# Kernel optimization log

Hardware: AMD Instinct MI355X
Metric: run time of the kernel (lower is better)

Reference implementation:

```python
import jax, jax.numpy as jnp
import numpy as np

B, S, D, H = 2, 4096, 512, 8
DK = D // H  # 64

def setup_inputs() -> dict:
    key = jax.random.key(0)
    k1, k2, k3, k4 = jax.random.split(key, 4)
    return {
        "queries": jax.random.normal(k1, (B, S, D), dtype=jnp.float32),
        "keys": jax.random.normal(k2, (B, S, D), dtype=jnp.float32),
        "values": jax.random.normal(k3, (B, S, D), dtype=jnp.float32),
        "W_o": jax.random.normal(k4, (D, D), dtype=jnp.float32) * (1.0 / np.sqrt(D)),
        "b_o": jnp.zeros((D,), dtype=jnp.float32),
    }

def reference(queries, keys, values, W_o, b_o):
    b_s, nq, _ = queries.shape
    nk = keys.shape[1]
    # split heads: (b, s, h, dk) -> (b, h, s, dk)
    q = queries.reshape(b_s, nq, H, DK).transpose(0, 2, 1, 3)
    k = keys.reshape(b_s, nk, H, DK).transpose(0, 2, 1, 3)
    v = values.reshape(b_s, nk, H, DK).transpose(0, 2, 1, 3)
    # full (nq, nk) attention matrix, scaled by sqrt(d_k)
    att = jnp.einsum("bhqd,bhkd->bhqk", q, k) / np.sqrt(DK).astype(np.float32)
    att = jax.nn.softmax(att, axis=-1)  # dropout is identity at inference
    out = jnp.einsum("bhqk,bhkd->bhqd", att, v)
    out = out.transpose(0, 2, 1, 3).reshape(b_s, nq, H * DK)
    return out @ W_o + b_o
```

## Files before the change

### kernel.cpp

```cpp
#include <hip/hip_runtime.h>
#include <hip/hip_bf16.h>

#define Bn 2
#define Sn 4096
#define Dn 512
#define Hn 8

typedef _Float16 f16x8 __attribute__((ext_vector_type(8)));
typedef __fp16 fp16x2 __attribute__((ext_vector_type(2)));
typedef float f32x16 __attribute__((ext_vector_type(16)));
typedef unsigned uint2v __attribute__((ext_vector_type(2)));

#if __has_builtin(__builtin_amdgcn_global_load_lds)
#define HAS_GLL 1
typedef const __attribute__((address_space(1))) unsigned int* gas1_t;
typedef __attribute__((address_space(3))) unsigned int* las3_t;
static __device__ __forceinline__ void ld_lds16(const void* g, void* l) {
    __builtin_amdgcn_global_load_lds((gas1_t)g, (las3_t)l, 16, 0, 0);
}
#else
#define HAS_GLL 0
#endif

static __device__ __forceinline__ unsigned pkh(float a, float b) {
    union { fp16x2 h; unsigned u; } r;
    r.h = __builtin_amdgcn_cvt_pkrtz(a, b);
    return r.u;
}

static __device__ __forceinline__ f16x8 xchg2(unsigned g0x, unsigned g0y,
                                              unsigned g1x, unsigned g1y, int hi) {
    union { unsigned u[4]; f16x8 v; } f;
#if __has_builtin(__builtin_amdgcn_permlane32_swap)
    uint2v rx = __builtin_amdgcn_permlane32_swap(g0x, g1x, false, false);
    uint2v ry = __builtin_amdgcn_permlane32_swap(g0y, g1y, false, false);
    f.u[0] = rx.x; f.u[1] = ry.x; f.u[2] = rx.y; f.u[3] = ry.y;
#else
    int sx = hi ? (int)g0x : (int)g1x;
    int sy = hi ? (int)g0y : (int)g1y;
    int rx = __shfl_xor(sx, 32);
    int ry = __shfl_xor(sy, 32);
    unsigned ox = hi ? g1x : g0x;
    unsigned oy = hi ? g1y : g0y;
    f.u[0] = hi ? (unsigned)rx : ox;
    f.u[1] = hi ? (unsigned)ry : oy;
    f.u[2] = hi ? ox : (unsigned)rx;
    f.u[3] = hi ? oy : (unsigned)ry;
#endif
    return f.v;
}

__global__ __launch_bounds__(256) void prep_kernel(
    const float* __restrict__ K, const float* __restrict__ V, const float* __restrict__ W,
    unsigned short* __restrict__ Kb, unsigned short* __restrict__ Vb,
    unsigned short* __restrict__ Wb) {
    const int vb = blockIdx.x;
    const int tid = threadIdx.x;
    if (vb < 1024) {
        const int kt = vb & 63, bh = vb >> 6;
        const int b = bh >> 3, h = bh & 7;
        unsigned short* dst = Kb + ((size_t)bh * 64 + kt) * 4096;
#pragma unroll
        for (int i = 0; i < 2; ++i) {
            int c = tid + i * 256;
            int f = c >> 6, ln = c & 63;
            int ktile = f >> 2, ks = f & 3;
            int row = ktile * 32 + (ln & 31);
            int dk = ks * 16 + (ln >> 5) * 8;
            const float* src = K + ((size_t)(b * Sn + kt * 64 + row)) * Dn + h * 64 + dk;
            float4 a0 = *(const float4*)src;
            float4 a1 = *(const float4*)(src + 4);
            uint4 o;
            o.x = pkh(a0.x, a0.y); o.y = pkh(a0.z, a0.w);
            o.z = pkh(a1.x, a1.y); o.w = pkh(a1.z, a1.w);
            *(uint4*)(dst + c * 8) = o;
        }
    } else if (vb < 2048) {
        const int u = vb - 1024;
        const int kt = u & 63, bh = u >> 6;
        const int b = bh >> 3, h = bh & 7;
        unsigned short* dst = Vb + ((size_t)bh * 64 + kt) * 4096;
#pragma unroll
        for (int i = 0; i < 2; ++i) {
            int c = tid + i * 256;
            int f = c >> 6, ln = c & 63;
            int dt = f >> 2, ks = f & 3;
            int dk = dt * 32 + (ln & 31);
            int key0 = ks * 16 + (ln >> 5) * 8;
            const float* src = V + ((size_t)(b * Sn + kt * 64 + key0)) * Dn + h * 64 + dk;
            uint4 o;
            o.x = pkh(src[0 * Dn], src[1 * Dn]);
            o.y = pkh(src[2 * Dn], src[3 * Dn]);
            o.z = pkh(src[4 * Dn], src[5 * Dn]);
            o.w = pkh(src[6 * Dn], src[7 * Dn]);
            *(uint4*)(dst + c * 8) = o;
        }
    } else {
        int c = (vb - 2048) * 256 + tid;
        int ln = c & 63, f = c >> 6;
        int ntile = f >> 5, ks = f & 31;
        int n = ntile * 32 + (ln & 31);
        int k0 = ks * 16 + (ln >> 5) * 8;
        uint4 o;
        o.x = pkh(W[(size_t)(k0 + 0) * Dn + n], W[(size_t)(k0 + 1) * Dn + n]);
        o.y = pkh(W[(size_t)(k0 + 2) * Dn + n], W[(size_t)(k0 + 3) * Dn + n]);
        o.z = pkh(W[(size_t)(k0 + 4) * Dn + n], W[(size_t)(k0 + 5) * Dn + n]);
        o.w = pkh(W[(size_t)(k0 + 6) * Dn + n], W[(size_t)(k0 + 7) * Dn + n]);
        *(uint4*)(Wb + c * 8) = o;
    }
}

__global__ __launch_bounds__(256, 2) void attn_kernel(
    const float* __restrict__ Q,
    const unsigned short* __restrict__ Kb,
    const unsigned short* __restrict__ Vb,
    unsigned short* __restrict__ ObA) {
    __shared__ __align__(16) unsigned short KV[32768];

    const int qt = blockIdx.x;
    const int bh = blockIdx.y;
    const int b = bh >> 3, h = bh & 7;
    const int tid = threadIdx.x;
    const int wg = tid >> 6;
    const int half = wg >> 1;
    const int qs = wg & 1;
    const int lane = tid & 63;
    const int q = lane & 31;
    const int hi = lane >> 5;
    const float cexp = 0.18033688f;

    f16x8 qf0[4], qf1[4];
    {
        const float* qp0 = Q + ((size_t)(b * Sn + qt * 128 + qs * 64 + q)) * Dn + h * 64 + hi * 8;
        const float* qp1 = qp0 + (size_t)32 * Dn;
#pragma unroll
        for (int ks = 0; ks < 4; ++ks) {
            float4 a0 = *(const float4*)(qp0 + ks * 16);
            float4 a1 = *(const float4*)(qp0 + ks * 16 + 4);
            union { unsigned u[4]; f16x8 v; } f;
            f.u[0] = pkh(a0.x * cexp, a0.y * cexp);
            f.u[1] = pkh(a0.z * cexp, a0.w * cexp);
            f.u[2] = pkh(a1.x * cexp, a1.y * cexp);
            f.u[3] = pkh(a1.z * cexp, a1.w * cexp);
            qf0[ks] = f.v;
            a0 = *(const float4*)(qp1 + ks * 16);
            a1 = *(const float4*)(qp1 + ks * 16 + 4);
            f.u[0] = pkh(a0.x * cexp, a0.y * cexp);
            f.u[1] = pkh(a0.z * cexp, a0.w * cexp);
            f.u[2] = pkh(a1.x * cexp, a1.y * cexp);
            f.u[3] = pkh(a1.z * cexp, a1.w * cexp);
            qf1[ks] = f.v;
        }
    }

    f32x16 zf;
#pragma unroll
    for (int r = 0; r < 16; ++r) zf[r] = 0.f;
    f32x16 oacc[2][2];
    oacc[0][0] = zf; oacc[0][1] = zf; oacc[1][0] = zf; oacc[1][1] = zf;
    float l0_ = 0.f, l1_ = 0.f;

    const size_t tbase = ((size_t)bh * 64 + half * 32) * 4096;
    const unsigned short* sgw = (qs ? Vb : Kb) + tbase;
    unsigned short* const lbase = &KV[half * 8192 + qs * 4096];

#if HAS_GLL
#define STAGE(itx, bb) { \
    const unsigned short* sp = sgw + (size_t)(itx) * 4096 + lane * 8; \
    unsigned short* ld = lbase + (bb) * 16384; \
    _Pragma("unroll") \
    for (int c = 0; c < 8; ++c) ld_lds16(sp + c * 512, ld + c * 512); }
#else
#define STAGE(itx, bb) { \
    const unsigned short* sp = sgw + (size_t)(itx) * 4096 + lane * 8; \
    unsigned short* ld = lbase + (bb) * 16384; \
    _Pragma("unroll") \
    for (int c = 0; c < 8; ++c) { \
        uint4 a = *(const uint4*)(sp + c * 512); \
        *(uint4*)&ld[c * 512 + lane * 8] = a; } }
#endif

    STAGE(0, 0);

    for (int it = 0; it < 32; ++it) {
        __syncthreads();
        const unsigned short* Kbuf = &KV[(it & 1) * 16384 + half * 8192];
        const unsigned short* Vbuf = Kbuf + 4096;
        if (it < 31) STAGE(it + 1, (it + 1) & 1);

#pragma unroll
        for (int kt2 = 0; kt2 < 2; ++kt2) {
            f32x16 sa0, sa1;
            {
                f16x8 kf = *(const f16x8*)&Kbuf[(kt2 * 4 + 0) * 512 + lane * 8];
                sa0 = __builtin_amdgcn_mfma_f32_32x32x16_f16(kf, qf0[0], zf, 0, 0, 0);
                sa1 = __builtin_amdgcn_mfma_f32_32x32x16_f16(kf, qf1[0], zf, 0, 0, 0);
#pragma unroll
                for (int ks = 1; ks < 4; ++ks) {
                    kf = *(const f16x8*)&Kbuf[(kt2 * 4 + ks) * 512 + lane * 8];
                    sa0 = __builtin_amdgcn_mfma_f32_32x32x16_f16(kf, qf0[ks], sa0, 0, 0, 0);
                    sa1 = __builtin_amdgcn_mfma_f32_32x32x16_f16(kf, qf1[ks], sa1, 0, 0, 0);
                }
            }
            unsigned u0[8], u1[8];
            float s0 = 0.f, s1 = 0.f;
#pragma unroll
            for (int j = 0; j < 8; ++j) {
                float ea = __builtin_amdgcn_exp2f(sa0[2 * j]);
                float eb = __builtin_amdgcn_exp2f(sa0[2 * j + 1]);
                s0 += ea + eb;
                u0[j] = pkh(ea, eb);
            }
#pragma unroll
            for (int j = 0; j < 8; ++j) {
                float ea = __builtin_amdgcn_exp2f(sa1[2 * j]);
                float eb = __builtin_amdgcn_exp2f(sa1[2 * j + 1]);
                s1 += ea + eb;
                u1[j] = pkh(ea, eb);
            }
            l0_ += s0; l1_ += s1;

#pragma unroll
            for (int kp = 0; kp < 2; ++kp) {
                f16x8 pb0 = xchg2(u0[4 * kp + 0], u0[4 * kp + 1], u0[4 * kp + 2], u0[4 * kp + 3], hi);
                f16x8 pb1 = xchg2(u1[4 * kp + 0], u1[4 * kp + 1], u1[4 * kp + 2], u1[4 * kp + 3], hi);
                f16x8 va0 = *(const f16x8*)&Vbuf[(0 * 4 + kt2 * 2 + kp) * 512 + lane * 8];
                f16x8 va1 = *(const f16x8*)&Vbuf[(1 * 4 + kt2 * 2 + kp) * 512 + lane * 8];
                oacc[0][0] = __builtin_amdgcn_mfma_f32_32x32x16_f16(va0, pb0, oacc[0][0], 0, 0, 0);
                oacc[0][1] = __builtin_amdgcn_mfma_f32_32x32x16_f16(va1, pb0, oacc[0][1], 0, 0, 0);
                oacc[1][0] = __builtin_amdgcn_mfma_f32_32x32x16_f16(va0, pb1, oacc[1][0], 0, 0, 0);
                oacc[1][1] = __builtin_amdgcn_mfma_f32_32x32x16_f16(va1, pb1, oacc[1][1], 0, 0, 0);
            }
        }
    }

    __syncthreads();
    float* red = (float*)KV + qs * 4224;
    if (half) {
#pragma unroll
        for (int t = 0; t < 2; ++t)
#pragma unroll
            for (int dt = 0; dt < 2; ++dt)
#pragma unroll
                for (int g = 0; g < 4; ++g) {
                    float4 v;
                    v.x = oacc[t][dt][g * 4 + 0];
                    v.y = oacc[t][dt][g * 4 + 1];
                    v.z = oacc[t][dt][g * 4 + 2];
                    v.w = oacc[t][dt][g * 4 + 3];
                    *(float4*)&red[((t * 2 + dt) * 4 + g) * 256 + lane * 4] = v;
                }
        red[4096 + lane] = l0_;
        red[4096 + 64 + lane] = l1_;
    }
    __syncthreads();
    if (!half) {
#pragma unroll
        for (int t = 0; t < 2; ++t)
#pragma unroll
            for (int dt = 0; dt < 2; ++dt)
#pragma unroll
                for (int g = 0; g < 4; ++g) {
                    float4 v = *(const float4*)&red[((t * 2 + dt) * 4 + g) * 256 + lane * 4];
                    oacc[t][dt][g * 4 + 0] += v.x;
                    oacc[t][dt][g * 4 + 1] += v.y;
                    oacc[t][dt][g * 4 + 2] += v.z;
                    oacc[t][dt][g * 4 + 3] += v.w;
                }
        l0_ += red[4096 + lane];
        l1_ += red[4096 + 64 + lane];
        l0_ += __shfl_xor(l0_, 32);
        l1_ += __shfl_xor(l1_, 32);
#pragma unroll
        for (int t = 0; t < 2; ++t) {
            const float li = 1.f / (t ? l1_ : l0_);
            const int gm = b * 128 + qt * 4 + qs * 2 + t;
#pragma unroll
            for (int ksg = 0; ksg < 4; ++ksg) {
                const int dt = ksg >> 1, k2 = ksg & 1;
                unsigned g0x = pkh(oacc[t][dt][8 * k2 + 0] * li, oacc[t][dt][8 * k2 + 1] * li);
                unsigned g0y = pkh(oacc[t][dt][8 * k2 + 2] * li, oacc[t][dt][8 * k2 + 3] * li);
                unsigned g1x = pkh(oacc[t][dt][8 * k2 + 4] * li, oacc[t][dt][8 * k2 + 5] * li);
                unsigned g1y = pkh(oacc[t][dt][8 * k2 + 6] * li, oacc[t][dt][8 * k2 + 7] * li);
                f16x8 frag = xchg2(g0x, g0y, g1x, g1y, hi);
                union { f16x8 v; uint4 u; } fu; fu.v = frag;
                *(uint4*)&ObA[((size_t)(gm * 32 + h * 4 + ksg) * 64 + lane) * 8] = fu.u;
            }
        }
    }
}

__global__ __launch_bounds__(256) void proj_kernel(
    const unsigned short* __restrict__ ObA,
    const unsigned short* __restrict__ Wb,
    const float* __restrict__ bias,
    float* __restrict__ out) {
    __shared__ __align__(16) unsigned short Ash[8192];
    __shared__ __align__(16) unsigned short Wsh[4096];

    const int mt = blockIdx.x;
    const int nt = blockIdx.y;
    const int tid = threadIdx.x;
    const int w = tid >> 6;
    const int lane = tid & 63;
    const int q = lane & 31;
    const int hi = lane >> 5;

    f32x16 acc[2];
#pragma unroll
    for (int t = 0; t < 2; ++t)
#pragma unroll
        for (int r = 0; r < 16; ++r) acc[t][r] = 0.f;

    for (int kt = 0; kt < 8; ++kt) {
        __syncthreads();
#pragma unroll
        for (int i = 0; i < 4; ++i) {
            int ci = (tid >> 6) + i * 4;
            int ml = ci >> 2, ksl = ci & 3;
            *(uint4*)&Ash[ci * 512 + lane * 8] =
                *(const uint4*)(ObA + (((size_t)(mt * 4 + ml) * 32 + kt * 4 + ksl) * 64 + lane) * 8);
        }
#pragma unroll
        for (int i = 0; i < 2; ++i) {
            int ci = (tid >> 6) + i * 4;
            int ntl = ci >> 2, ksl = ci & 3;
            *(uint4*)&Wsh[ci * 512 + lane * 8] =
                *(const uint4*)(Wb + (((size_t)(nt * 2 + ntl) * 32 + kt * 4 + ksl) * 64 + lane) * 8);
        }
        __syncthreads();

#pragma unroll
        for (int ks = 0; ks < 4; ++ks) {
            f16x8 a  = *(const f16x8*)&Ash[(w * 4 + ks) * 512 + lane * 8];
            f16x8 b0 = *(const f16x8*)&Wsh[(0 * 4 + ks) * 512 + lane * 8];
            f16x8 b1 = *(const f16x8*)&Wsh[(4 + ks) * 512 + lane * 8];
            acc[0] = __builtin_amdgcn_mfma_f32_32x32x16_f16(a, b0, acc[0], 0, 0, 0);
            acc[1] = __builtin_amdgcn_mfma_f32_32x32x16_f16(a, b1, acc[1], 0, 0, 0);
        }
    }

#pragma unroll
    for (int ntl = 0; ntl < 2; ++ntl) {
        int col = nt * 64 + ntl * 32 + q;
        float bv = bias[col];
#pragma unroll
        for (int reg = 0; reg < 16; ++reg) {
            int row = mt * 128 + w * 32 + (reg & 3) + 8 * (reg >> 2) + 4 * hi;
            out[(size_t)row * Dn + col] = acc[ntl][reg] + bv;
        }
    }
}

extern "C" void kernel_launch(void* const* d_in, const int* in_sizes, int n_in,
                              void* d_out, int out_size, void* d_ws, size_t ws_size,
                              hipStream_t stream) {
    const float* Q = (const float*)d_in[0];
    const float* K = (const float*)d_in[1];
    const float* V = (const float*)d_in[2];
    const float* W = (const float*)d_in[3];
    const float* bo = (const float*)d_in[4];
    float* out = (float*)d_out;

    char* ws = (char*)d_ws;
    unsigned short* Kb  = (unsigned short*)(ws);
    unsigned short* Vb  = (unsigned short*)(ws + 8388608);
    unsigned short* Wb  = (unsigned short*)(ws + 16777216);
    unsigned short* ObA = (unsigned short*)(ws + 17301504);

    prep_kernel<<<2176, 256, 0, stream>>>(K, V, W, Kb, Vb, Wb);
    attn_kernel<<<dim3(32, 16), 256, 0, stream>>>(Q, Kb, Vb, ObA);
    proj_kernel<<<dim3(64, 8), 256, 0, stream>>>(ObA, Wb, bo, out);
}
```

Baseline: 178.0 us.

## Split attention KV sequence across four wave pairs with 512-thread blocks

Doubles the attention block to 512 threads so that four key groups, instead of two, each process a quarter of the KV sequence for the same 128-query tile. Each iteration now handles 32 keys per group, and the partial outputs are reduced through LDS in two passes, one per query sub-tile, with extra barriers. Block indices are also remapped so consecutive blocks share query tiles across heads, and launch bounds ask for 4 blocks per CU. The aim is more waves in flight per CU to hide latency, at the cost of smaller MFMA batches per barrier and a larger reduction step.

```diff
diff --git a/kernel.cpp b/kernel.cpp
--- a/kernel.cpp
+++ b/kernel.cpp
@@ -110,19 +110,20 @@
     }
 }
 
-__global__ __launch_bounds__(256, 2) void attn_kernel(
+__global__ __launch_bounds__(512, 4) void attn_kernel(
     const float* __restrict__ Q,
     const unsigned short* __restrict__ Kb,
     const unsigned short* __restrict__ Vb,
     unsigned short* __restrict__ ObA) {
     __shared__ __align__(16) unsigned short KV[32768];
 
-    const int qt = blockIdx.x;
-    const int bh = blockIdx.y;
+    const int id = blockIdx.x + (blockIdx.y << 5);
+    const int qt = (id >> 3) & 31;
+    const int bh = (id & 7) + ((id >> 8) << 3);
     const int b = bh >> 3, h = bh & 7;
     const int tid = threadIdx.x;
     const int wg = tid >> 6;
-    const int half = wg >> 1;
+    const int kg = wg >> 1;
     const int qs = wg & 1;
     const int lane = tid & 63;
     const int q = lane & 31;
@@ -160,85 +161,101 @@
     oacc[0][0] = zf; oacc[0][1] = zf; oacc[1][0] = zf; oacc[1][1] = zf;
     float l0_ = 0.f, l1_ = 0.f;
 
-    const size_t tbase = ((size_t)bh * 64 + half * 32) * 4096;
-    const unsigned short* sgw = (qs ? Vb : Kb) + tbase;
-    unsigned short* const lbase = &KV[half * 8192 + qs * 4096];
+    const size_t bhbase = (size_t)bh * 64 * 4096;
 
 #if HAS_GLL
 #define STAGE(itx, bb) { \
-    const unsigned short* sp = sgw + (size_t)(itx) * 4096 + lane * 8; \
-    unsigned short* ld = lbase + (bb) * 16384; \
-    _Pragma("unroll") \
-    for (int c = 0; c < 8; ++c) ld_lds16(sp + c * 512, ld + c * 512); }
+    const int t64 = kg * 16 + ((itx) >> 1); \
+    const int lohi = (itx) & 1; \
+    unsigned short* dst = &KV[(bb) * 16384 + kg * 4096]; \
+    if (qs == 0) { \
+        const unsigned short* sp = Kb + bhbase + (size_t)t64 * 4096 + lohi * 2048 + lane * 8; \
+        ld_lds16(sp, dst); ld_lds16(sp + 512, dst + 512); \
+        ld_lds16(sp + 1024, dst + 1024); ld_lds16(sp + 1536, dst + 1536); \
+    } else { \
+        const unsigned short* sp = Vb + bhbase + (size_t)t64 * 4096 + lohi * 1024 + lane * 8; \
+        unsigned short* dv = dst + 2048; \
+        ld_lds16(sp, dv); ld_lds16(sp + 512, dv + 512); \
+        ld_lds16(sp + 2048, dv + 1024); ld_lds16(sp + 2560, dv + 1536); \
+    } }
 #else
 #define STAGE(itx, bb) { \
-    const unsigned short* sp = sgw + (size_t)(itx) * 4096 + lane * 8; \
-    unsigned short* ld = lbase + (bb) * 16384; \
-    _Pragma("unroll") \
-    for (int c = 0; c < 8; ++c) { \
-        uint4 a = *(const uint4*)(sp + c * 512); \
-        *(uint4*)&ld[c * 512 + lane * 8] = a; } }
+    const int t64 = kg * 16 + ((itx) >> 1); \
+    const int lohi = (itx) & 1; \
+    unsigned short* dst = &KV[(bb) * 16384 + kg * 4096]; \
+    if (qs == 0) { \
+        const unsigned short* sp = Kb + bhbase + (size_t)t64 * 4096 + lohi * 2048 + lane * 8; \
+        uint4 a0 = *(const uint4*)(sp); uint4 a1 = *(const uint4*)(sp + 512); \
+        uint4 a2 = *(const uint4*)(sp + 1024); uint4 a3 = *(const uint4*)(sp + 1536); \
+        *(uint4*)&dst[lane * 8] = a0; *(uint4*)&dst[512 + lane * 8] = a1; \
+        *(uint4*)&dst[1024 + lane * 8] = a2; *(uint4*)&dst[1536 + lane * 8] = a3; \
+    } else { \
+        const unsigned short* sp = Vb + bhbase + (size_t)t64 * 4096 + lohi * 1024 + lane * 8; \
+        unsigned short* dv = dst + 2048; \
+        uint4 a0 = *(const uint4*)(sp); uint4 a1 = *(const uint4*)(sp + 512); \
+        uint4 a2 = *(const uint4*)(sp + 2048); uint4 a3 = *(const uint4*)(sp + 2560); \
+        *(uint4*)&dv[lane * 8] = a0; *(uint4*)&dv[512 + lane * 8] = a1; \
+        *(uint4*)&dv[1024 + lane * 8] = a2; *(uint4*)&dv[1536 + lane * 8] = a3; \
+    } }
 #endif
 
     STAGE(0, 0);
 
     for (int it = 0; it < 32; ++it) {
         __syncthreads();
-        const unsigned short* Kbuf = &KV[(it & 1) * 16384 + half * 8192];
-        const unsigned short* Vbuf = Kbuf + 4096;
+        const unsigned short* Kbuf = &KV[(it & 1) * 16384 + kg * 4096];
+        const unsigned short* Vbuf = Kbuf + 2048;
         if (it < 31) STAGE(it + 1, (it + 1) & 1);
 
-#pragma unroll
-        for (int kt2 = 0; kt2 < 2; ++kt2) {
-            f32x16 sa0, sa1;
-            {
-                f16x8 kf = *(const f16x8*)&Kbuf[(kt2 * 4 + 0) * 512 + lane * 8];
-                sa0 = __builtin_amdgcn_mfma_f32_32x32x16_f16(kf, qf0[0], zf, 0, 0, 0);
-                sa1 = __builtin_amdgcn_mfma_f32_32x32x16_f16(kf, qf1[0], zf, 0, 0, 0);
-#pragma unroll
-                for (int ks = 1; ks < 4; ++ks) {
-                    kf = *(const f16x8*)&Kbuf[(kt2 * 4 + ks) * 512 + lane * 8];
-                    sa0 = __builtin_amdgcn_mfma_f32_32x32x16_f16(kf, qf0[ks], sa0, 0, 0, 0);
-                    sa1 = __builtin_amdgcn_mfma_f32_32x32x16_f16(kf, qf1[ks], sa1, 0, 0, 0);
-                }
+        f32x16 sa0, sa1;
+        {
+            f16x8 kf = *(const f16x8*)&Kbuf[0 * 512 + lane * 8];
+            sa0 = __builtin_amdgcn_mfma_f32_32x32x16_f16(kf, qf0[0], zf, 0, 0, 0);
+            sa1 = __builtin_amdgcn_mfma_f32_32x32x16_f16(kf, qf1[0], zf, 0, 0, 0);
+#pragma unroll
+            for (int ks = 1; ks < 4; ++ks) {
+                kf = *(const f16x8*)&Kbuf[ks * 512 + lane * 8];
+                sa0 = __builtin_amdgcn_mfma_f32_32x32x16_f16(kf, qf0[ks], sa0, 0, 0, 0);
+                sa1 = __builtin_amdgcn_mfma_f32_32x32x16_f16(kf, qf1[ks], sa1, 0, 0, 0);
             }
-            unsigned u0[8], u1[8];
-            float s0 = 0.f, s1 = 0.f;
-#pragma unroll
-            for (int j = 0; j < 8; ++j) {
-                float ea = __builtin_amdgcn_exp2f(sa0[2 * j]);
-                float eb = __builtin_amdgcn_exp2f(sa0[2 * j + 1]);
-                s0 += ea + eb;
-                u0[j] = pkh(ea, eb);
-            }
-#pragma unroll
-            for (int j = 0; j < 8; ++j) {
-                float ea = __builtin_amdgcn_exp2f(sa1[2 * j]);
-                float eb = __builtin_amdgcn_exp2f(sa1[2 * j + 1]);
-                s1 += ea + eb;
-                u1[j] = pkh(ea, eb);
-            }
-            l0_ += s0; l1_ += s1;
-
-#pragma unroll
-            for (int kp = 0; kp < 2; ++kp) {
-                f16x8 pb0 = xchg2(u0[4 * kp + 0], u0[4 * kp + 1], u0[4 * kp + 2], u0[4 * kp + 3], hi);
-                f16x8 pb1 = xchg2(u1[4 * kp + 0], u1[4 * kp + 1], u1[4 * kp + 2], u1[4 * kp + 3], hi);
-                f16x8 va0 = *(const f16x8*)&Vbuf[(0 * 4 + kt2 * 2 + kp) * 512 + lane * 8];
-                f16x8 va1 = *(const f16x8*)&Vbuf[(1 * 4 + kt2 * 2 + kp) * 512 + lane * 8];
-                oacc[0][0] = __builtin_amdgcn_mfma_f32_32x32x16_f16(va0, pb0, oacc[0][0], 0, 0, 0);
-                oacc[0][1] = __builtin_amdgcn_mfma_f32_32x32x16_f16(va1, pb0, oacc[0][1], 0, 0, 0);
-                oacc[1][0] = __builtin_amdgcn_mfma_f32_32x32x16_f16(va0, pb1, oacc[1][0], 0, 0, 0);
-                oacc[1][1] = __builtin_amdgcn_mfma_f32_32x32x16_f16(va1, pb1, oacc[1][1], 0, 0, 0);
-            }
+        }
+        unsigned u0[8], u1[8];
+        float s0 = 0.f, s1 = 0.f;
+#pragma unroll
+        for (int j = 0; j < 8; ++j) {
+            float ea = __builtin_amdgcn_exp2f(sa0[2 * j]);
+            float eb = __builtin_amdgcn_exp2f(sa0[2 * j + 1]);
+            s0 += ea + eb;
+            u0[j] = pkh(ea, eb);
+        }
+#pragma unroll
+        for (int j = 0; j < 8; ++j) {
+            float ea = __builtin_amdgcn_exp2f(sa1[2 * j]);
+            float eb = __builtin_amdgcn_exp2f(sa1[2 * j + 1]);
+            s1 += ea + eb;
+            u1[j] = pkh(ea, eb);
+        }
+        l0_ += s0; l1_ += s1;
+
+#pragma unroll
+        for (int ks2 = 0; ks2 < 2; ++ks2) {
+            f16x8 pb0 = xchg2(u0[4 * ks2 + 0], u0[4 * ks2 + 1], u0[4 * ks2 + 2], u0[4 * ks2 + 3], hi);
+            f16x8 pb1 = xchg2(u1[4 * ks2 + 0], u1[4 * ks2 + 1], u1[4 * ks2 + 2], u1[4 * ks2 + 3], hi);
+            f16x8 va0 = *(const f16x8*)&Vbuf[ks2 * 512 + lane * 8];
+            f16x8 va1 = *(const f16x8*)&Vbuf[1024 + ks2 * 512 + lane * 8];
+            oacc[0][0] = __builtin_amdgcn_mfma_f32_32x32x16_f16(va0, pb0, oacc[0][0], 0, 0, 0);
+            oacc[0][1] = __builtin_amdgcn_mfma_f32_32x32x16_f16(va1, pb0, oacc[0][1], 0, 0, 0);
+            oacc[1][0] = __builtin_amdgcn_mfma_f32_32x32x16_f16(va0, pb1, oacc[1][0], 0, 0, 0);
+            oacc[1][1] = __builtin_amdgcn_mfma_f32_32x32x16_f16(va1, pb1, oacc[1][1], 0, 0, 0);
         }
     }
 
     __syncthreads();
-    float* red = (float*)KV + qs * 4224;
-    if (half) {
-#pragma unroll
-        for (int t = 0; t < 2; ++t)
+    float* red = (float*)KV;
+#pragma unroll
+    for (int t = 0; t < 2; ++t) {
+        if (kg != 0) {
+            float* rp = red + (qs * 3 + (kg - 1)) * 2048;
 #pragma unroll
             for (int dt = 0; dt < 2; ++dt)
 #pragma unroll
@@ -248,27 +265,33 @@
                     v.y = oacc[t][dt][g * 4 + 1];
                     v.z = oacc[t][dt][g * 4 + 2];
                     v.w = oacc[t][dt][g * 4 + 3];
-                    *(float4*)&red[((t * 2 + dt) * 4 + g) * 256 + lane * 4] = v;
+                    *(float4*)&rp[(dt * 4 + g) * 256 + lane * 4] = v;
                 }
-        red[4096 + lane] = l0_;
-        red[4096 + 64 + lane] = l1_;
-    }
-    __syncthreads();
-    if (!half) {
-#pragma unroll
-        for (int t = 0; t < 2; ++t)
-#pragma unroll
-            for (int dt = 0; dt < 2; ++dt)
-#pragma unroll
-                for (int g = 0; g < 4; ++g) {
-                    float4 v = *(const float4*)&red[((t * 2 + dt) * 4 + g) * 256 + lane * 4];
-                    oacc[t][dt][g * 4 + 0] += v.x;
-                    oacc[t][dt][g * 4 + 1] += v.y;
-                    oacc[t][dt][g * 4 + 2] += v.z;
-                    oacc[t][dt][g * 4 + 3] += v.w;
-                }
-        l0_ += red[4096 + lane];
-        l1_ += red[4096 + 64 + lane];
+            red[12288 + (qs * 3 + (kg - 1)) * 64 + lane] = t ? l1_ : l0_;
+        }
+        __syncthreads();
+        if (kg == 0) {
+#pragma unroll
+            for (int slot = 0; slot < 3; ++slot) {
+                float* rp = red + (qs * 3 + slot) * 2048;
+#pragma unroll
+                for (int dt = 0; dt < 2; ++dt)
+#pragma unroll
+                    for (int g = 0; g < 4; ++g) {
+                        float4 v = *(const float4*)&rp[(dt * 4 + g) * 256 + lane * 4];
+                        oacc[t][dt][g * 4 + 0] += v.x;
+                        oacc[t][dt][g * 4 + 1] += v.y;
+                        oacc[t][dt][g * 4 + 2] += v.z;
+                        oacc[t][dt][g * 4 + 3] += v.w;
+                    }
+                float addl = red[12288 + (qs * 3 + slot) * 64 + lane];
+                if (t) l1_ += addl; else l0_ += addl;
+            }
+        }
+        __syncthreads();
+    }
+
+    if (kg == 0) {
         l0_ += __shfl_xor(l0_, 32);
         l1_ += __shfl_xor(l1_, 32);
 #pragma unroll
@@ -369,6 +392,6 @@
     unsigned short* ObA = (unsigned short*)(ws + 17301504);
 
     prep_kernel<<<2176, 256, 0, stream>>>(K, V, W, Kb, Vb, Wb);
-    attn_kernel<<<dim3(32, 16), 256, 0, stream>>>(Q, Kb, Vb, ObA);
+    attn_kernel<<<dim3(32, 16), 512, 0, stream>>>(Q, Kb, Vb, ObA);
     proj_kernel<<<dim3(64, 8), 256, 0, stream>>>(ObA, Wb, bo, out);
 }
```

Result: slower. 641.9 us (+260.6%).
